# Performance work log

Hardware: AMD Instinct MI355X
Metric: run time of the kernel (lower is better)

Reference implementation:

```python
import jax, jax.numpy as jnp
import numpy as np

B, H, FEAT = 16384, 256, 256
GX, GY, SW = 70, 70, 2


def setup_inputs() -> dict:
    key = jax.random.key(0)
    ks = jax.random.split(key, 10)
    stdv = 1.0 / np.sqrt(H)
    feats = jax.random.normal(ks[0], (B, FEAT), dtype=jnp.float32)
    coords = jax.random.randint(ks[1], (B, 2), 0, 64).astype(jnp.float32)
    input_tensor = jnp.concatenate([feats, coords], axis=1)  # [B, FEAT+2]
    hidden = jax.random.normal(ks[2], (B, H), dtype=jnp.float32)
    u = lambda k, shp: jax.random.uniform(k, shp, jnp.float32, -stdv, stdv)
    return {
        "input_tensor": input_tensor,
        "hidden": hidden,
        "w_ih": u(ks[3], (4 * H, FEAT)),
        "b_ih": u(ks[4], (4 * H,)),
        "w_hh": u(ks[5], (4 * H, H)),
        "b_hh": u(ks[6], (4 * H,)),
        "w_out": u(ks[7], (H, 2 * H)),
        "b_out": u(ks[8], (H,)),
        "memory": jax.random.normal(ks[9], (GX, GY, H), dtype=jnp.float32) * 0.1,
    }


def reference(input_tensor, hidden, w_ih, b_ih, w_hh, b_hh, w_out, b_out, memory):
    feature = input_tensor[:, :-2]
    grid = input_tensor[:, -2:].astype(jnp.int32) + SW  # [B,2]

    gi = feature @ w_ih.T + b_ih  # [B,4H]
    gh = hidden @ w_hh.T + b_hh   # [B,4H]
    i_r, i_i, i_n, i_s = jnp.split(gi, 4, axis=1)
    h_r, h_i, h_n, h_s = jnp.split(gh, 4, axis=1)

    resetgate = jax.nn.sigmoid(i_r + h_r)
    updategate = jax.nn.sigmoid(i_i + h_i)
    spatialgate = jax.nn.sigmoid(i_s + h_s)
    newgate = jnp.tanh(i_n + resetgate * h_n)

    # gather (2*SW+1)^2 neighborhood per sample from spatial memory
    gx = jnp.clip(grid[:, 0], 0, GX - 1)
    gy = jnp.clip(grid[:, 1], 0, GY - 1)
    off = jnp.arange(-SW, SW + 1)  # [K]
    xi = jnp.clip(gx[:, None] + off[None, :], 0, GX - 1)  # [B,K]
    yi = jnp.clip(gy[:, None] + off[None, :], 0, GY - 1)  # [B,K]
    K = 2 * SW + 1
    x_flat = jnp.broadcast_to(xi[:, :, None], (xi.shape[0], K, K)).reshape(xi.shape[0], -1)
    y_flat = jnp.broadcast_to(yi[:, None, :], (yi.shape[0], K, K)).reshape(yi.shape[0], -1)
    context = memory[x_flat, y_flat]  # [B, K*K, H]

    # attention (query is detached in original)
    q = jax.lax.stop_gradient(newgate)  # [B,H]
    attn = jnp.einsum('bh,bkh->bk', q, context)  # [B, K*K]
    attn = jnp.where(attn == 0, -jnp.inf, attn)
    w = jax.nn.softmax(attn, axis=1)
    w = jnp.where(jnp.isnan(w), 0.0, w)
    mix = jnp.einsum('bk,bkh->bh', w, context)  # [B,H]
    combined = jnp.concatenate([mix, q], axis=1)  # [B,2H]
    atten_cs = jnp.tanh(combined @ w_out.T + b_out)  # [B,H]

    curr_state = newgate + spatialgate * atten_cs
    output = curr_state + updategate * (hidden - curr_state)
    return output
```

## Files before the change

kernel.cpp:

```cpp
#include <hip/hip_runtime.h>
#include <stdint.h>

#define B_N 16384
#define H_N 256
#define IN_W 258
#define GX_N 70
#define GY_N 70
#define SW_N 2
#define KK_N 25

typedef __bf16 bf16x8 __attribute__((ext_vector_type(8)));
typedef __bf16 bf16x4 __attribute__((ext_vector_type(4)));
typedef __bf16 bf16x2 __attribute__((ext_vector_type(2)));
typedef float f32x4 __attribute__((ext_vector_type(4)));
typedef float f32x2 __attribute__((ext_vector_type(2)));

#define AS1 __attribute__((address_space(1)))
#define AS3 __attribute__((address_space(3)))

static __device__ __forceinline__ void gload16(const void* g, void* l) {
    __builtin_amdgcn_global_load_lds((const AS1 uint32_t*)g, (AS3 uint32_t*)l, 16, 0, 0);
}

#define E_AB   8388608ULL
#define E_WF   8912896ULL
#define E_WOUT 9043968ULL
#define E_COMB 9043968ULL
#define E_UGSG 17432576ULL

__global__ __launch_bounds__(256) void cast_kernel(
    const float* __restrict__ in_t, const float* __restrict__ hid,
    const float* __restrict__ wih, const float* __restrict__ whh,
    const float* __restrict__ wout, __bf16* __restrict__ dst)
{
    size_t g = (size_t)blockIdx.x * blockDim.x + threadIdx.x;
    size_t stride = (size_t)gridDim.x * blockDim.x;
    for (size_t e = g * 8; e < E_WOUT; e += stride * 8) {
        float s[8];
        if (e < E_AB) {
            size_t row = e >> 9;
            size_t c = e & 511;
            if (c < 256) {
                const f32x2* s2 = reinterpret_cast<const f32x2*>(in_t + row * IN_W + c);
#pragma unroll
                for (int q = 0; q < 4; q++) { f32x2 a = s2[q]; s[q * 2] = a.x; s[q * 2 + 1] = a.y; }
            } else {
                const f32x4* s4 = reinterpret_cast<const f32x4*>(hid + row * 256 + (c - 256));
#pragma unroll
                for (int q = 0; q < 2; q++) { f32x4 a = s4[q]; s[q*4]=a.x; s[q*4+1]=a.y; s[q*4+2]=a.z; s[q*4+3]=a.w; }
            }
        } else if (e < E_WF) {
            size_t off = e - E_AB;
            size_t j = off >> 9;
            size_t k = off & 511;
            size_t c = j >> 8;
            size_t col = j & 255;
            size_t base = (c == 0) ? 0 : (c == 1) ? 256 : (c == 2) ? 768 : 512;
            const float* srcm = (k < 256) ? wih : whh;
            const f32x4* s4 = reinterpret_cast<const f32x4*>(srcm + (base + col) * 256 + (k & 255));
#pragma unroll
            for (int q = 0; q < 2; q++) { f32x4 a = s4[q]; s[q*4]=a.x; s[q*4+1]=a.y; s[q*4+2]=a.z; s[q*4+3]=a.w; }
        } else {
            const f32x4* s4 = reinterpret_cast<const f32x4*>(wout + (e - E_WF));
#pragma unroll
            for (int q = 0; q < 2; q++) { f32x4 a = s4[q]; s[q*4]=a.x; s[q*4+1]=a.y; s[q*4+2]=a.z; s[q*4+3]=a.w; }
        }
        bf16x8 o;
#pragma unroll
        for (int q = 0; q < 8; q++) o[q] = (__bf16)s[q];
        *reinterpret_cast<bf16x8*>(dst + e) = o;
    }
}

__global__ __launch_bounds__(256, 2) void gates_gemm(
    const __bf16* __restrict__ AB, const __bf16* __restrict__ wfull,
    const float* __restrict__ b_ih, const float* __restrict__ b_hh,
    __bf16* __restrict__ comb, __bf16* __restrict__ ugsg)
{
    __shared__ __bf16 ldsA[2][4096];
    __shared__ __bf16 ldsB[2][4096];
    const int t = threadIdx.x;
    const int lane = t & 63, w = t >> 6;
    const int lr = lane & 15, seg = lane >> 4;
    const int rb = blockIdx.x * 128;
    const int h0 = blockIdx.y * 32;

    const int rA = t & 127;
    const int sA = t >> 7;
    const __bf16* gAt = AB + (size_t)(rb + rA) * 512 + sA * 8;
    const int bc = rA >> 5, bcol = rA & 31;
    const __bf16* gBt = wfull + (size_t)(bc * 256 + h0 + bcol) * 512 + sA * 8;
    __bf16* lA0 = &ldsA[0][t * 8];
    __bf16* lA1 = &ldsA[1][t * 8];
    __bf16* lB0 = &ldsB[0][t * 8];
    __bf16* lB1 = &ldsB[1][t * 8];

    f32x4 acc[2][6], accni[2][2], accnh[2][2];
#pragma unroll
    for (int rh = 0; rh < 2; rh++) {
#pragma unroll
        for (int cn = 0; cn < 6; cn++) acc[rh][cn] = (f32x4){0.f, 0.f, 0.f, 0.f};
        accni[rh][0] = (f32x4){0.f, 0.f, 0.f, 0.f};
        accni[rh][1] = (f32x4){0.f, 0.f, 0.f, 0.f};
        accnh[rh][0] = (f32x4){0.f, 0.f, 0.f, 0.f};
        accnh[rh][1] = (f32x4){0.f, 0.f, 0.f, 0.f};
    }

    gload16(gAt + 0, lA0);
    gload16(gAt + 16, lA0 + 2048);
    gload16(gBt + 0, lB0);
    gload16(gBt + 16, lB0 + 2048);
    __syncthreads();

#pragma unroll 1
    for (int tt = 0; tt < 16; tt++) {
        const int cur = tt & 1;
        if (tt < 15) {
            const int kn = (tt + 1) * 32;
            __bf16* la = cur ? lA0 : lA1;
            __bf16* lb = cur ? lB0 : lB1;
            gload16(gAt + kn, la);
            gload16(gAt + kn + 16, la + 2048);
            gload16(gBt + kn, lb);
            gload16(gBt + kn + 16, lb + 2048);
        }
        const __bf16* cA = ldsA[cur];
        const __bf16* cB = ldsB[cur];
        bf16x8 af[2];
#pragma unroll
        for (int rh = 0; rh < 2; rh++)
            af[rh] = *reinterpret_cast<const bf16x8*>(cA + seg * 1024 + (w * 32 + rh * 16 + lr) * 8);
#pragma unroll
        for (int cn = 0; cn < 6; cn++) {
            const int c = cn >> 1, hh = cn & 1;
            bf16x8 bb = *reinterpret_cast<const bf16x8*>(cB + seg * 1024 + (c * 32 + hh * 16 + lr) * 8);
#pragma unroll
            for (int rh = 0; rh < 2; rh++)
                acc[rh][(c << 1) + hh] = __builtin_amdgcn_mfma_f32_16x16x32_bf16(af[rh], bb, acc[rh][(c << 1) + hh], 0, 0, 0);
        }
        bf16x8 b6 = *reinterpret_cast<const bf16x8*>(cB + seg * 1024 + (96 + lr) * 8);
        bf16x8 b7 = *reinterpret_cast<const bf16x8*>(cB + seg * 1024 + (112 + lr) * 8);
        if (tt < 8) {
#pragma unroll
            for (int rh = 0; rh < 2; rh++) {
                accni[rh][0] = __builtin_amdgcn_mfma_f32_16x16x32_bf16(af[rh], b6, accni[rh][0], 0, 0, 0);
                accni[rh][1] = __builtin_amdgcn_mfma_f32_16x16x32_bf16(af[rh], b7, accni[rh][1], 0, 0, 0);
            }
        } else {
#pragma unroll
            for (int rh = 0; rh < 2; rh++) {
                accnh[rh][0] = __builtin_amdgcn_mfma_f32_16x16x32_bf16(af[rh], b6, accnh[rh][0], 0, 0, 0);
                accnh[rh][1] = __builtin_amdgcn_mfma_f32_16x16x32_bf16(af[rh], b7, accnh[rh][1], 0, 0, 0);
            }
        }
        __syncthreads();
    }

#pragma unroll
    for (int hh = 0; hh < 2; hh++) {
        const int col = h0 + hh * 16 + lr;
        const float br_ = b_ih[col] + b_hh[col];
        const float bi_ = b_ih[col + 256] + b_hh[col + 256];
        const float bs_ = b_ih[col + 768] + b_hh[col + 768];
        const float bni = b_ih[col + 512];
        const float bnh = b_hh[col + 512];
#pragma unroll
        for (int rh = 0; rh < 2; rh++) {
#pragma unroll
            for (int r = 0; r < 4; r++) {
                const int row = rb + w * 32 + rh * 16 + seg * 4 + r;
                float sr = acc[rh][hh][r] + br_;
                float si = acc[rh][2 + hh][r] + bi_;
                float ss = acc[rh][4 + hh][r] + bs_;
                float vni = accni[rh][hh][r] + bni;
                float vnh = accnh[rh][hh][r] + bnh;
                float rg = 1.f / (1.f + __expf(-sr));
                float ug = 1.f / (1.f + __expf(-si));
                float sg = 1.f / (1.f + __expf(-ss));
                float ng = tanhf(vni + rg * vnh);
                comb[(size_t)row * 512 + 256 + col] = (__bf16)ng;
                bf16x2 us;
                us.x = (__bf16)ug;
                us.y = (__bf16)sg;
                *reinterpret_cast<bf16x2*>(ugsg + ((size_t)row * 256 + col) * 2) = us;
            }
        }
    }
}

template <int CTRL>
static __device__ __forceinline__ float dpp_add_step(float x) {
    int xi = __builtin_bit_cast(int, x);
    int sh = __builtin_amdgcn_update_dpp(0, xi, CTRL, 0xf, 0xf, true);
    return x + __builtin_bit_cast(float, sh);
}
static __device__ __forceinline__ float wave_sum_readlane(float x) {
    x = dpp_add_step<0x111>(x);
    x = dpp_add_step<0x112>(x);
    x = dpp_add_step<0x114>(x);
    x = dpp_add_step<0x118>(x);
    x = dpp_add_step<0x142>(x);
    x = dpp_add_step<0x143>(x);
    int s = __builtin_amdgcn_readlane(__builtin_bit_cast(int, x), 63);
    return __builtin_bit_cast(float, s);
}

__global__ __launch_bounds__(256) void attn_kernel(
    const float* __restrict__ in_t, const float* __restrict__ memory,
    __bf16* __restrict__ comb)
{
    const int w = threadIdx.x >> 6;
    const int lane = threadIdx.x & 63;
    const int b = blockIdx.x * 4 + w;
    const float* row_in = in_t + (size_t)b * IN_W;
    int gx = (int)row_in[256] + SW_N;
    int gy = (int)row_in[257] + SW_N;
    gx = min(max(gx, 0), GX_N - 1);
    gy = min(max(gy, 0), GY_N - 1);

    int xs[5], ys[5];
#pragma unroll
    for (int d = 0; d < 5; d++) {
        xs[d] = min(max(gx + d - SW_N, 0), GX_N - 1);
        ys[d] = min(max(gy + d - SW_N, 0), GY_N - 1);
    }

    bf16x4 qb = *reinterpret_cast<const bf16x4*>(comb + (size_t)b * 512 + 256 + lane * 4);
    const float q0 = (float)qb.x, q1 = (float)qb.y, q2 = (float)qb.z, q3 = (float)qb.w;

    f32x4 v[KK_N];
    float sc[KK_N];
#pragma unroll
    for (int k = 0; k < KK_N; k++) {
        const int i = k / 5, j = k % 5;
        const f32x4* cp = reinterpret_cast<const f32x4*>(
            memory + ((size_t)xs[i] * GY_N + ys[j]) * H_N);
        v[k] = cp[lane];
        float p = q0 * v[k].x + q1 * v[k].y + q2 * v[k].z + q3 * v[k].w;
        sc[k] = wave_sum_readlane(p);
    }

#pragma unroll
    for (int k = 0; k < KK_N; k++) sc[k] = (sc[k] == 0.f) ? -INFINITY : sc[k];
    float mx = -INFINITY;
#pragma unroll
    for (int k = 0; k < KK_N; k++) mx = fmaxf(mx, sc[k]);
    float d = 0.f;
    if (mx > -INFINITY) {
#pragma unroll
        for (int k = 0; k < KK_N; k++) { sc[k] = __expf(sc[k] - mx); d += sc[k]; }
    } else {
#pragma unroll
        for (int k = 0; k < KK_N; k++) sc[k] = 0.f;
    }
    const float inv = (d != 0.f) ? 1.f / d : 0.f;

    f32x4 o = (f32x4){0.f, 0.f, 0.f, 0.f};
#pragma unroll
    for (int k = 0; k < KK_N; k++) {
        const float wk = sc[k] * inv;
        o.x += wk * v[k].x; o.y += wk * v[k].y; o.z += wk * v[k].z; o.w += wk * v[k].w;
    }
    bf16x4 ob;
    ob.x = (__bf16)o.x; ob.y = (__bf16)o.y; ob.z = (__bf16)o.z; ob.w = (__bf16)o.w;
    *reinterpret_cast<bf16x4*>(comb + (size_t)b * 512 + lane * 4) = ob;
}

__global__ __launch_bounds__(256, 4) void out_gemm(
    const __bf16* __restrict__ comb, const __bf16* __restrict__ woB,
    const float* __restrict__ b_out, const __bf16* __restrict__ ugsg,
    const float* __restrict__ hidden, float* __restrict__ out)
{
    __shared__ __bf16 ldsA[2][4096];
    __shared__ __bf16 ldsB[2][4096];
    const int t = threadIdx.x;
    const int lane = t & 63, w = t >> 6;
    const int lr = lane & 15, seg = lane >> 4;
    const int rb = blockIdx.x * 64;
    const int n0 = blockIdx.y * 64;

    const __bf16* gAt = comb + (size_t)(rb + (t & 63)) * 512 + ((t >> 6) << 3);
    const __bf16* gBt = woB + (size_t)(n0 + (t & 63)) * 512 + ((t >> 6) << 3);
    __bf16* lA0 = &ldsA[0][t * 8];
    __bf16* lA1 = &ldsA[1][t * 8];
    __bf16* lB0 = &ldsB[0][t * 8];
    __bf16* lB1 = &ldsB[1][t * 8];

    f32x4 acc[4];
#pragma unroll
    for (int ct = 0; ct < 4; ct++) acc[ct] = (f32x4){0.f, 0.f, 0.f, 0.f};

    gload16(gAt + 0, lA0);
    gload16(gAt + 32, lA0 + 2048);
    gload16(gBt + 0, lB0);
    gload16(gBt + 32, lB0 + 2048);
    __syncthreads();

#pragma unroll 1
    for (int tt = 0; tt < 8; tt++) {
        const int cur = tt & 1;
        if (tt < 7) {
            const int kn = (tt + 1) * 64;
            __bf16* la = cur ? lA0 : lA1;
            __bf16* lb = cur ? lB0 : lB1;
            gload16(gAt + kn, la);
            gload16(gAt + kn + 32, la + 2048);
            gload16(gBt + kn, lb);
            gload16(gBt + kn + 32, lb + 2048);
        }
        const __bf16* cA = ldsA[cur];
        const __bf16* cB = ldsB[cur];
        bf16x8 af[2];
#pragma unroll
        for (int kb = 0; kb < 2; kb++)
            af[kb] = *reinterpret_cast<const bf16x8*>(cA + kb * 2048 + seg * 512 + (w * 16 + lr) * 8);
#pragma unroll
        for (int ct = 0; ct < 4; ct++) {
#pragma unroll
            for (int kb = 0; kb < 2; kb++) {
                bf16x8 bb = *reinterpret_cast<const bf16x8*>(cB + kb * 2048 + seg * 512 + (ct * 16 + lr) * 8);
                acc[ct] = __builtin_amdgcn_mfma_f32_16x16x32_bf16(af[kb], bb, acc[ct], 0, 0, 0);
            }
        }
        __syncthreads();
    }

#pragma unroll
    for (int ct = 0; ct < 4; ct++) {
        int col = n0 + ct * 16 + lr;
        float bo = b_out[col];
#pragma unroll
        for (int r = 0; r < 4; r++) {
            int row = rb + w * 16 + seg * 4 + r;
            size_t idx = (size_t)row * 256 + col;
            float acs = tanhf(acc[ct][r] + bo);
            float ng = (float)comb[(size_t)row * 512 + 256 + col];
            bf16x2 us = *reinterpret_cast<const bf16x2*>(ugsg + idx * 2);
            float ug = (float)us.x, sg = (float)us.y;
            float curr = ng + sg * acs;
            out[idx] = curr + ug * (hidden[idx] - curr);
        }
    }
}

extern "C" void kernel_launch(void* const* d_in, const int* in_sizes, int n_in,
                              void* d_out, int out_size, void* d_ws, size_t ws_size,
                              hipStream_t stream) {
    const float* input_t = (const float*)d_in[0];
    const float* hidden  = (const float*)d_in[1];
    const float* w_ih    = (const float*)d_in[2];
    const float* b_ih    = (const float*)d_in[3];
    const float* w_hh    = (const float*)d_in[4];
    const float* b_hh    = (const float*)d_in[5];
    const float* w_out   = (const float*)d_in[6];
    const float* b_out   = (const float*)d_in[7];
    const float* memory  = (const float*)d_in[8];
    float* out = (float*)d_out;

    __bf16* base  = (__bf16*)d_ws;
    __bf16* AB    = base;
    __bf16* wfull = base + E_AB;
    __bf16* woutB = base + E_WF;
    __bf16* comb  = base + E_COMB;
    __bf16* ugsg  = base + E_UGSG;

    cast_kernel<<<4096, 256, 0, stream>>>(input_t, hidden, w_ih, w_hh, w_out, base);
    gates_gemm<<<dim3(128, 8), 256, 0, stream>>>(AB, wfull, b_ih, b_hh, comb, ugsg);
    attn_kernel<<<4096, 256, 0, stream>>>(input_t, memory, comb);
    out_gemm<<<dim3(256, 4), 256, 0, stream>>>(comb, woutB, b_out, ugsg, hidden, out);
}
```

Measured before the change: 190.8 us.

## Fuse activation fp32-to-bf16 cast into gates GEMM A-tile loading

Removes the pre-pass that converted input features and hidden state to a bf16 workspace buffer. The gates GEMM now reads fp32 activations straight into registers, converts them, and writes them to LDS after the MFMA work for the current tile. The cast kernel now handles only the weights and uses fewer blocks. This avoids a full write and re-read of the 16 MB bf16 activation copy, at the cost of each of the 8 column blocks reading fp32 A (twice the bytes), plus extra registers and conversion work inside the GEMM loop.

```diff
diff --git a/kernel.cpp b/kernel.cpp
--- a/kernel.cpp
+++ b/kernel.cpp
@@ -12,6 +12,7 @@
 typedef __bf16 bf16x8 __attribute__((ext_vector_type(8)));
 typedef __bf16 bf16x4 __attribute__((ext_vector_type(4)));
 typedef __bf16 bf16x2 __attribute__((ext_vector_type(2)));
+typedef float f32x8 __attribute__((ext_vector_type(8)));
 typedef float f32x4 __attribute__((ext_vector_type(4)));
 typedef float f32x2 __attribute__((ext_vector_type(2)));
 
@@ -29,27 +30,14 @@
 #define E_UGSG 17432576ULL
 
 __global__ __launch_bounds__(256) void cast_kernel(
-    const float* __restrict__ in_t, const float* __restrict__ hid,
     const float* __restrict__ wih, const float* __restrict__ whh,
     const float* __restrict__ wout, __bf16* __restrict__ dst)
 {
     size_t g = (size_t)blockIdx.x * blockDim.x + threadIdx.x;
     size_t stride = (size_t)gridDim.x * blockDim.x;
-    for (size_t e = g * 8; e < E_WOUT; e += stride * 8) {
-        float s[8];
-        if (e < E_AB) {
-            size_t row = e >> 9;
-            size_t c = e & 511;
-            if (c < 256) {
-                const f32x2* s2 = reinterpret_cast<const f32x2*>(in_t + row * IN_W + c);
-#pragma unroll
-                for (int q = 0; q < 4; q++) { f32x2 a = s2[q]; s[q * 2] = a.x; s[q * 2 + 1] = a.y; }
-            } else {
-                const f32x4* s4 = reinterpret_cast<const f32x4*>(hid + row * 256 + (c - 256));
-#pragma unroll
-                for (int q = 0; q < 2; q++) { f32x4 a = s4[q]; s[q*4]=a.x; s[q*4+1]=a.y; s[q*4+2]=a.z; s[q*4+3]=a.w; }
-            }
-        } else if (e < E_WF) {
+    for (size_t e = E_AB + g * 8; e < E_WOUT; e += stride * 8) {
+        const float* src;
+        if (e < E_WF) {
             size_t off = e - E_AB;
             size_t j = off >> 9;
             size_t k = off & 511;
@@ -57,23 +45,46 @@
             size_t col = j & 255;
             size_t base = (c == 0) ? 0 : (c == 1) ? 256 : (c == 2) ? 768 : 512;
             const float* srcm = (k < 256) ? wih : whh;
-            const f32x4* s4 = reinterpret_cast<const f32x4*>(srcm + (base + col) * 256 + (k & 255));
-#pragma unroll
-            for (int q = 0; q < 2; q++) { f32x4 a = s4[q]; s[q*4]=a.x; s[q*4+1]=a.y; s[q*4+2]=a.z; s[q*4+3]=a.w; }
+            src = srcm + (base + col) * 256 + (k & 255);
         } else {
-            const f32x4* s4 = reinterpret_cast<const f32x4*>(wout + (e - E_WF));
-#pragma unroll
-            for (int q = 0; q < 2; q++) { f32x4 a = s4[q]; s[q*4]=a.x; s[q*4+1]=a.y; s[q*4+2]=a.z; s[q*4+3]=a.w; }
-        }
+            src = wout + (e - E_WF);
+        }
+        const f32x4* s4 = reinterpret_cast<const f32x4*>(src);
+        f32x4 a = s4[0], b = s4[1];
         bf16x8 o;
-#pragma unroll
-        for (int q = 0; q < 8; q++) o[q] = (__bf16)s[q];
+        o[0] = (__bf16)a.x; o[1] = (__bf16)a.y; o[2] = (__bf16)a.z; o[3] = (__bf16)a.w;
+        o[4] = (__bf16)b.x; o[5] = (__bf16)b.y; o[6] = (__bf16)b.z; o[7] = (__bf16)b.w;
         *reinterpret_cast<bf16x8*>(dst + e) = o;
     }
 }
 
+static __device__ __forceinline__ f32x8 loadA8(
+    const float* __restrict__ featp, const float* __restrict__ hidp, int k0)
+{
+    f32x8 r;
+    if (k0 < 256) {
+        const f32x2* p = reinterpret_cast<const f32x2*>(featp + k0);
+        f32x2 a = p[0], b = p[1], c = p[2], d = p[3];
+        r[0] = a.x; r[1] = a.y; r[2] = b.x; r[3] = b.y;
+        r[4] = c.x; r[5] = c.y; r[6] = d.x; r[7] = d.y;
+    } else {
+        const f32x4* p = reinterpret_cast<const f32x4*>(hidp + (k0 - 256));
+        f32x4 a = p[0], b = p[1];
+        r[0] = a.x; r[1] = a.y; r[2] = a.z; r[3] = a.w;
+        r[4] = b.x; r[5] = b.y; r[6] = b.z; r[7] = b.w;
+    }
+    return r;
+}
+static __device__ __forceinline__ void cvtStore(__bf16* dst, f32x8 v) {
+    bf16x8 o;
+#pragma unroll
+    for (int q = 0; q < 8; q++) o[q] = (__bf16)v[q];
+    *reinterpret_cast<bf16x8*>(dst) = o;
+}
+
 __global__ __launch_bounds__(256, 2) void gates_gemm(
-    const __bf16* __restrict__ AB, const __bf16* __restrict__ wfull,
+    const float* __restrict__ in_t, const float* __restrict__ hid,
+    const __bf16* __restrict__ wfull,
     const float* __restrict__ b_ih, const float* __restrict__ b_hh,
     __bf16* __restrict__ comb, __bf16* __restrict__ ugsg)
 {
@@ -87,7 +98,8 @@
 
     const int rA = t & 127;
     const int sA = t >> 7;
-    const __bf16* gAt = AB + (size_t)(rb + rA) * 512 + sA * 8;
+    const float* featp = in_t + (size_t)(rb + rA) * IN_W;
+    const float* hidp  = hid + (size_t)(rb + rA) * 256;
     const int bc = rA >> 5, bcol = rA & 31;
     const __bf16* gBt = wfull + (size_t)(bc * 256 + h0 + bcol) * 512 + sA * 8;
     __bf16* lA0 = &ldsA[0][t * 8];
@@ -106,23 +118,27 @@
         accnh[rh][1] = (f32x4){0.f, 0.f, 0.f, 0.f};
     }
 
-    gload16(gAt + 0, lA0);
-    gload16(gAt + 16, lA0 + 2048);
     gload16(gBt + 0, lB0);
     gload16(gBt + 16, lB0 + 2048);
+    {
+        f32x8 a0 = loadA8(featp, hidp, sA * 8);
+        f32x8 a1 = loadA8(featp, hidp, sA * 8 + 16);
+        cvtStore(lA0, a0);
+        cvtStore(lA0 + 2048, a1);
+    }
     __syncthreads();
 
 #pragma unroll 1
     for (int tt = 0; tt < 16; tt++) {
         const int cur = tt & 1;
+        f32x8 a0, a1;
         if (tt < 15) {
             const int kn = (tt + 1) * 32;
-            __bf16* la = cur ? lA0 : lA1;
             __bf16* lb = cur ? lB0 : lB1;
-            gload16(gAt + kn, la);
-            gload16(gAt + kn + 16, la + 2048);
             gload16(gBt + kn, lb);
             gload16(gBt + kn + 16, lb + 2048);
+            a0 = loadA8(featp, hidp, kn + sA * 8);
+            a1 = loadA8(featp, hidp, kn + sA * 8 + 16);
         }
         const __bf16* cA = ldsA[cur];
         const __bf16* cB = ldsB[cur];
@@ -152,6 +168,11 @@
                 accnh[rh][0] = __builtin_amdgcn_mfma_f32_16x16x32_bf16(af[rh], b6, accnh[rh][0], 0, 0, 0);
                 accnh[rh][1] = __builtin_amdgcn_mfma_f32_16x16x32_bf16(af[rh], b7, accnh[rh][1], 0, 0, 0);
             }
+        }
+        if (tt < 15) {
+            __bf16* la = cur ? lA0 : lA1;
+            cvtStore(la, a0);
+            cvtStore(la + 2048, a1);
         }
         __syncthreads();
     }
@@ -358,14 +379,13 @@
     float* out = (float*)d_out;
 
     __bf16* base  = (__bf16*)d_ws;
-    __bf16* AB    = base;
     __bf16* wfull = base + E_AB;
     __bf16* woutB = base + E_WF;
     __bf16* comb  = base + E_COMB;
     __bf16* ugsg  = base + E_UGSG;
 
-    cast_kernel<<<4096, 256, 0, stream>>>(input_t, hidden, w_ih, w_hh, w_out, base);
-    gates_gemm<<<dim3(128, 8), 256, 0, stream>>>(AB, wfull, b_ih, b_hh, comb, ugsg);
+    cast_kernel<<<320, 256, 0, stream>>>(w_ih, w_hh, w_out, base);
+    gates_gemm<<<dim3(128, 8), 256, 0, stream>>>(input_t, hidden, wfull, b_ih, b_hh, comb, ugsg);
     attn_kernel<<<4096, 256, 0, stream>>>(input_t, memory, comb);
     out_gemm<<<dim3(256, 4), 256, 0, stream>>>(comb, woutB, b_out, ugsg, hidden, out);
 }
```

After: 207.4 us. 8.7% more time.
